# Performance work log

Hardware: AMD Instinct MI355X
Metric: run time of the kernel (lower is better)

## Reference

```python
import jax, jax.numpy as jnp
import numpy as np

WINDOW_SIZE = 20
NEG_BIG = -1e8  # matches -10**8 in the torch mask


def band_mask(S):
    # 0 inside the sliding window |i-j| <= WINDOW_SIZE, -1e8 outside (additive mask)
    idx = jnp.arange(S)
    return jnp.where(jnp.abs(idx[:, None] - idx[None, :]) <= WINDOW_SIZE, 0.0, NEG_BIG).astype(jnp.float32)


def setup_inputs() -> dict:
    key = jax.random.key(0)
    k1, k2, k3, k4 = jax.random.split(key, 4)
    B, S, Dq, Dk = 8, 2048, 1024, 1024
    queries = jax.random.normal(k1, (B, S, Dq), dtype=jnp.float32)
    keys = jax.random.normal(k2, (B, S, Dk), dtype=jnp.float32)
    # reduce = nn.Linear(key_dim, query_dim) since key_dim >= query_dim
    lim = 1.0 / np.sqrt(Dk)
    W_reduce = jax.random.uniform(k3, (Dq, Dk), jnp.float32, -lim, lim)
    b_reduce = jax.random.uniform(k4, (Dq,), jnp.float32, -lim, lim)
    return {"queries": queries, "keys": keys, "W_reduce": W_reduce, "b_reduce": b_reduce}


def reference(queries, keys, W_reduce, b_reduce):
    # values default to the ORIGINAL keys (before dim matching)
    values = keys
    # match_dims: reduce keys to query_dim
    keys_r = jnp.einsum('bkd,qd->bkq', keys, W_reduce) + b_reduce  # [B,S,Dq]
    sims = jnp.einsum('bqd,bkd->bqk', queries, keys_r)             # [B,S,S]
    sims = sims + band_mask(queries.shape[1])                      # additive banded window mask
    weights = jax.nn.softmax(sims, axis=-1)
    return jnp.einsum('bqk,bkd->bqd', weights, values)
```

## Files before the change

kernel.cpp:

```cpp
#include <hip/hip_runtime.h>


#define BATCH 8
#define SEQ   2048
#define DIM   1024
#define WIN   20

typedef _Float16 half8 __attribute__((ext_vector_type(8)));
typedef _Float16 half4v __attribute__((ext_vector_type(4)));
typedef float    f32x4 __attribute__((ext_vector_type(4)));

#define LDK 40

__global__ __launch_bounds__(256) void gemm_qw_f16(const float* __restrict__ Q,
                                                   const float* __restrict__ W,
                                                   float* __restrict__ QT) {
    __shared__ _Float16 Asl[128 * LDK];
    __shared__ _Float16 Bsl[128 * LDK];

    const int m0 = blockIdx.x * 128;
    const int n0 = blockIdx.y * 128;
    const int t  = threadIdx.x;
    const int lane = t & 63;
    const int wv   = t >> 6;
    const int wm   = (wv >> 1) * 64;
    const int wn   = (wv & 1) * 64;
    const int l15  = lane & 15;
    const int quad = lane >> 4;

    const int ar = t >> 1;
    const int ac = (t & 1) * 16;
    const float* Aptr = Q + (size_t)(m0 + ar) * DIM + ac;
    _Float16* AsW = &Asl[ar * LDK + ac];

    const int br = t >> 3;
    const int bc = t & 7;
    const float* Bptr = W + (size_t)br * DIM + n0 + bc;

    f32x4 acc[4][4] = {};

    for (int k0 = 0; k0 < DIM; k0 += 32) {
        float4 a0 = *(const float4*)(Aptr + k0);
        float4 a1 = *(const float4*)(Aptr + k0 + 4);
        float4 a2 = *(const float4*)(Aptr + k0 + 8);
        float4 a3 = *(const float4*)(Aptr + k0 + 12);
        float bv[16];
        #pragma unroll
        for (int j = 0; j < 16; ++j) bv[j] = Bptr[(size_t)k0 * DIM + 8 * j];

        __syncthreads();

        half8 h0, h1;
        h0[0] = (_Float16)a0.x; h0[1] = (_Float16)a0.y; h0[2] = (_Float16)a0.z; h0[3] = (_Float16)a0.w;
        h0[4] = (_Float16)a1.x; h0[5] = (_Float16)a1.y; h0[6] = (_Float16)a1.z; h0[7] = (_Float16)a1.w;
        h1[0] = (_Float16)a2.x; h1[1] = (_Float16)a2.y; h1[2] = (_Float16)a2.z; h1[3] = (_Float16)a2.w;
        h1[4] = (_Float16)a3.x; h1[5] = (_Float16)a3.y; h1[6] = (_Float16)a3.z; h1[7] = (_Float16)a3.w;
        *(half8*)(AsW)     = h0;
        *(half8*)(AsW + 8) = h1;

        #pragma unroll
        for (int j = 0; j < 16; ++j)
            Bsl[(bc + 8 * j) * LDK + br] = (_Float16)bv[j];

        __syncthreads();

        half8 af[4], bf[4];
        #pragma unroll
        for (int i = 0; i < 4; ++i)
            af[i] = *(const half8*)&Asl[(wm + i * 16 + l15) * LDK + quad * 8];
        #pragma unroll
        for (int j = 0; j < 4; ++j)
            bf[j] = *(const half8*)&Bsl[(wn + j * 16 + l15) * LDK + quad * 8];

        #pragma unroll
        for (int i = 0; i < 4; ++i)
            #pragma unroll
            for (int j = 0; j < 4; ++j)
                acc[i][j] = __builtin_amdgcn_mfma_f32_16x16x32_f16(af[i], bf[j], acc[i][j], 0, 0, 0);
    }

    #pragma unroll
    for (int i = 0; i < 4; ++i) {
        const int row0 = m0 + wm + i * 16 + quad * 4;
        #pragma unroll
        for (int r = 0; r < 4; ++r) {
            float* orow = QT + (size_t)(row0 + r) * DIM + n0 + wn + l15;
            #pragma unroll
            for (int j = 0; j < 4; ++j)
                orow[j * 16] = acc[i][j][r];
        }
    }
}

#define TQ  16
#define KP  64
#define KLD 80
#define QLD 80
#define SLD 66

__global__ __launch_bounds__(256, 4) void attn_mfma(const float* __restrict__ QT,
                                                    const float* __restrict__ Keys,
                                                    float* __restrict__ Out) {
    const int blk  = blockIdx.x;
    const int b    = blk & 7;
    const int tile = blk >> 3;
    const int q0   = tile * TQ;
    const int t    = threadIdx.x;
    const int lane = t & 63;
    const int wv   = t >> 6;
    const int l15  = lane & 15;
    const int quad = lane >> 4;

    const int klo = (q0 - WIN) > 0 ? (q0 - WIN) : 0;
    const int khi = (q0 + TQ - 1 + WIN) < (SEQ - 1) ? (q0 + TQ - 1 + WIN) : (SEQ - 1);
    const int nk  = khi - klo + 1;

    const float* qt   = QT + ((size_t)b * SEQ + q0) * DIM;
    const float* keys = Keys + (size_t)b * SEQ * DIM;

    __shared__ _Float16 Qc[TQ * QLD];
    __shared__ _Float16 Ks[KP * KLD];
    __shared__ float    Sl[TQ * SLD];
    __shared__ float    Wl[TQ * SLD];

    const int qr = t >> 4;
    const int qc = (t & 15) * 4;
    const int kr = t >> 2;
    const int kc = (t & 3) * 4;
    const int krow = (klo + kr) < (SEQ - 1) ? (klo + kr) : (SEQ - 1);

    const float* qsrc = qt + (size_t)qr * DIM + qc;
    const float* ksrc = keys + (size_t)krow * DIM + kc;

    f32x4 acc_s = {};

    for (int d0 = 0; d0 < DIM; d0 += 64) {
        float4 qv  = *(const float4*)(qsrc + d0);
        float4 kv0 = *(const float4*)(ksrc + d0);
        float4 kv1 = *(const float4*)(ksrc + d0 + 16);
        float4 kv2 = *(const float4*)(ksrc + d0 + 32);
        float4 kv3 = *(const float4*)(ksrc + d0 + 48);

        __syncthreads();

        half4v hq = {(_Float16)qv.x, (_Float16)qv.y, (_Float16)qv.z, (_Float16)qv.w};
        *(half4v*)&Qc[qr * QLD + qc] = hq;
        half4v h0 = {(_Float16)kv0.x, (_Float16)kv0.y, (_Float16)kv0.z, (_Float16)kv0.w};
        half4v h1 = {(_Float16)kv1.x, (_Float16)kv1.y, (_Float16)kv1.z, (_Float16)kv1.w};
        half4v h2 = {(_Float16)kv2.x, (_Float16)kv2.y, (_Float16)kv2.z, (_Float16)kv2.w};
        half4v h3 = {(_Float16)kv3.x, (_Float16)kv3.y, (_Float16)kv3.z, (_Float16)kv3.w};
        *(half4v*)&Ks[kr * KLD + kc]      = h0;
        *(half4v*)&Ks[kr * KLD + kc + 16] = h1;
        *(half4v*)&Ks[kr * KLD + kc + 32] = h2;
        *(half4v*)&Ks[kr * KLD + kc + 48] = h3;

        __syncthreads();

        #pragma unroll
        for (int s = 0; s < 2; ++s) {
            half8 af = *(const half8*)&Qc[l15 * QLD + s * 32 + quad * 8];
            half8 bf = *(const half8*)&Ks[(wv * 16 + l15) * KLD + s * 32 + quad * 8];
            acc_s = __builtin_amdgcn_mfma_f32_16x16x32_f16(af, bf, acc_s, 0, 0, 0);
        }
    }

    __syncthreads();
    #pragma unroll
    for (int r = 0; r < 4; ++r) {
        const int q = quad * 4 + r;
        const int c = wv * 16 + l15;
        const int d = (q0 + q) - (klo + c);
        const bool valid = (c < nk) && ((unsigned)(d + WIN) <= 2u * WIN);
        Sl[q * SLD + c] = valid ? acc_s[r] : -1e30f;
    }
    __syncthreads();

    if (t < 64) {
        const int q = t >> 2, part = t & 3;
        const float* srow = &Sl[q * SLD + part * 16];
        float*       wrow = &Wl[q * SLD + part * 16];
        float m = -1e30f;
        #pragma unroll
        for (int i = 0; i < 16; ++i) m = fmaxf(m, srow[i]);
        m = fmaxf(m, __shfl_xor(m, 1));
        m = fmaxf(m, __shfl_xor(m, 2));
        float ssum = 0.f;
        #pragma unroll
        for (int i = 0; i < 16; ++i) { float e = expf(srow[i] - m); wrow[i] = e; ssum += e; }
        ssum += __shfl_xor(ssum, 1);
        ssum += __shfl_xor(ssum, 2);
        const float inv = 1.f / ssum;
        #pragma unroll
        for (int i = 0; i < 16; ++i) wrow[i] *= inv;
    }
    __syncthreads();

    float accs[TQ][4] = {};
    for (int c = 0; c < nk; ++c) {
        const float* krow2 = keys + (size_t)(klo + c) * DIM;
        const float k0 = krow2[t], k1 = krow2[t + 256], k2 = krow2[t + 512], k3 = krow2[t + 768];
        #pragma unroll
        for (int q = 0; q < TQ; ++q) {
            const float w = Wl[q * SLD + c];
            accs[q][0] = fmaf(w, k0, accs[q][0]);
            accs[q][1] = fmaf(w, k1, accs[q][1]);
            accs[q][2] = fmaf(w, k2, accs[q][2]);
            accs[q][3] = fmaf(w, k3, accs[q][3]);
        }
    }
    #pragma unroll
    for (int q = 0; q < TQ; ++q) {
        float* orow = Out + ((size_t)b * SEQ + q0 + q) * DIM;
        orow[t]       = accs[q][0];
        orow[t + 256] = accs[q][1];
        orow[t + 512] = accs[q][2];
        orow[t + 768] = accs[q][3];
    }
}

extern "C" void kernel_launch(void* const* d_in, const int* in_sizes, int n_in,
                              void* d_out, int out_size, void* d_ws, size_t ws_size,
                              hipStream_t stream) {
    const float* queries = (const float*)d_in[0];
    const float* keys    = (const float*)d_in[1];
    const float* W       = (const float*)d_in[2];
    float* out = (float*)d_out;

    dim3 g1(128, 8);
    gemm_qw_f16<<<g1, 256, 0, stream>>>(queries, W, out);

    const int nblk = (BATCH * SEQ) / TQ;
    attn_mfma<<<nblk, 256, 0, stream>>>(out, keys, out);
}
```

Baseline: 286.9 us.

## Pre-convert Q and W to fp16 and use swizzled direct-to-LDS GEMM

Adds separate kernels that convert queries to fp16 and transpose-convert W to fp16. A new GEMM then loads both operands straight into LDS through global_load_lds with an XOR swizzle, and writes the Q·W product in fp16 into the workspace. The attention kernel is templated so it can read fp16 QT, which halves its Q traffic. The aim is to cut fp32 load bandwidth and the in-loop conversion and transpose cost in the GEMM. In exchange it adds two extra kernel launches and a full pass over Q, and the fp16 intermediate may cost precision. The old path is kept as a fallback when the workspace is too small.

```diff
diff --git a/kernel.cpp b/kernel.cpp
--- a/kernel.cpp
+++ b/kernel.cpp
@@ -6,12 +6,118 @@
 #define DIM   1024
 #define WIN   20
 
-typedef _Float16 half8 __attribute__((ext_vector_type(8)));
+typedef _Float16 half8  __attribute__((ext_vector_type(8)));
 typedef _Float16 half4v __attribute__((ext_vector_type(4)));
-typedef float    f32x4 __attribute__((ext_vector_type(4)));
+typedef float    f32x4  __attribute__((ext_vector_type(4)));
+
+#define GLOAD_LDS16(gsrc, ldst)                                                        \
+    __builtin_amdgcn_global_load_lds(                                                  \
+        (const __attribute__((address_space(1))) void*)(gsrc),                         \
+        (__attribute__((address_space(3))) void*)(ldst), 16, 0, 0)
+
+__global__ __launch_bounds__(256) void cvt_q_f16(const float* __restrict__ in,
+                                                 _Float16* __restrict__ out) {
+    const int n8 = (BATCH * SEQ * DIM) / 8;
+    for (int i = blockIdx.x * 256 + threadIdx.x; i < n8; i += gridDim.x * 256) {
+        const float4 a = ((const float4*)in)[2 * i];
+        const float4 b = ((const float4*)in)[2 * i + 1];
+        half8 h;
+        h[0] = (_Float16)a.x; h[1] = (_Float16)a.y; h[2] = (_Float16)a.z; h[3] = (_Float16)a.w;
+        h[4] = (_Float16)b.x; h[5] = (_Float16)b.y; h[6] = (_Float16)b.z; h[7] = (_Float16)b.w;
+        ((half8*)out)[i] = h;
+    }
+}
+
+#define WTS 68
+__global__ __launch_bounds__(256) void cvt_w_t(const float* __restrict__ W,
+                                               _Float16* __restrict__ WT) {
+    __shared__ _Float16 tile[64 * WTS];
+    const int k0 = blockIdx.x * 64;
+    const int n0 = blockIdx.y * 64;
+    const int t  = threadIdx.x;
+    const int r  = t >> 4;
+    const int c4 = (t & 15) * 4;
+    #pragma unroll
+    for (int rr = 0; rr < 64; rr += 16) {
+        float4 v = *(const float4*)&W[(size_t)(k0 + rr + r) * DIM + n0 + c4];
+        _Float16* dst = &tile[(rr + r) * WTS + c4];
+        dst[0] = (_Float16)v.x; dst[1] = (_Float16)v.y;
+        dst[2] = (_Float16)v.z; dst[3] = (_Float16)v.w;
+    }
+    __syncthreads();
+    #pragma unroll
+    for (int rr = 0; rr < 64; rr += 16) {
+        const int n = rr + r;
+        half4v h = { tile[(c4 + 0) * WTS + n], tile[(c4 + 1) * WTS + n],
+                     tile[(c4 + 2) * WTS + n], tile[(c4 + 3) * WTS + n] };
+        *(half4v*)&WT[(size_t)(n0 + n) * DIM + k0 + c4] = h;
+    }
+}
+
+#define GK 64
+__global__ __launch_bounds__(256, 2) void gemm_f16t(const _Float16* __restrict__ A,
+                                                    const _Float16* __restrict__ B,
+                                                    _Float16* __restrict__ C) {
+    __shared__ _Float16 As[128 * GK];
+    __shared__ _Float16 Bs[128 * GK];
+
+    const int m0   = blockIdx.x * 128;
+    const int n0   = blockIdx.y * 128;
+    const int t    = threadIdx.x;
+    const int lane = t & 63;
+    const int wv   = t >> 6;
+    const int wm   = (wv >> 1) * 64;
+    const int wn   = (wv & 1) * 64;
+    const int l15  = lane & 15;
+    const int quad = lane >> 4;
+
+    const int srow = lane >> 3;
+    const int sck  = (lane & 7) ^ srow;
+
+    f32x4 acc[4][4] = {};
+
+    for (int k0 = 0; k0 < DIM; k0 += GK) {
+        __syncthreads();
+        #pragma unroll
+        for (int j = 0; j < 4; ++j) {
+            const int rs = (j * 4 + wv) * 8;
+            GLOAD_LDS16(A + (size_t)(m0 + rs + srow) * DIM + k0 + sck * 8, &As[rs * GK]);
+            GLOAD_LDS16(B + (size_t)(n0 + rs + srow) * DIM + k0 + sck * 8, &Bs[rs * GK]);
+        }
+        __syncthreads();
+
+        #pragma unroll
+        for (int s = 0; s < 2; ++s) {
+            half8 af[4], bf[4];
+            #pragma unroll
+            for (int i = 0; i < 4; ++i)
+                af[i] = *(const half8*)&As[(wm + i * 16 + l15) * GK +
+                                           (((s * 4 + quad) ^ (l15 & 7)) * 8)];
+            #pragma unroll
+            for (int j = 0; j < 4; ++j)
+                bf[j] = *(const half8*)&Bs[(wn + j * 16 + l15) * GK +
+                                           (((s * 4 + quad) ^ (l15 & 7)) * 8)];
+            #pragma unroll
+            for (int i = 0; i < 4; ++i)
+                #pragma unroll
+                for (int j = 0; j < 4; ++j)
+                    acc[i][j] = __builtin_amdgcn_mfma_f32_16x16x32_f16(af[i], bf[j], acc[i][j], 0, 0, 0);
+        }
+    }
+
+    #pragma unroll
+    for (int i = 0; i < 4; ++i) {
+        #pragma unroll
+        for (int r = 0; r < 4; ++r) {
+            _Float16* crow = C + (size_t)(m0 + wm + i * 16 + quad * 4 + r) * DIM + n0 + wn + l15;
+            #pragma unroll
+            for (int j = 0; j < 4; ++j)
+                crow[j * 16] = (_Float16)acc[i][j][r];
+        }
+    }
+}
 
 #define LDK 40
-
 __global__ __launch_bounds__(256) void gemm_qw_f16(const float* __restrict__ Q,
                                                    const float* __restrict__ W,
                                                    float* __restrict__ QT) {
@@ -98,7 +204,8 @@
 #define QLD 80
 #define SLD 66
 
-__global__ __launch_bounds__(256, 4) void attn_mfma(const float* __restrict__ QT,
+template <typename QTT>
+__global__ __launch_bounds__(256, 4) void attn_mfma(const QTT* __restrict__ QT,
                                                     const float* __restrict__ Keys,
                                                     float* __restrict__ Out) {
     const int blk  = blockIdx.x;
@@ -115,7 +222,7 @@
     const int khi = (q0 + TQ - 1 + WIN) < (SEQ - 1) ? (q0 + TQ - 1 + WIN) : (SEQ - 1);
     const int nk  = khi - klo + 1;
 
-    const float* qt   = QT + ((size_t)b * SEQ + q0) * DIM;
+    const QTT*   qt   = QT + ((size_t)b * SEQ + q0) * DIM;
     const float* keys = Keys + (size_t)b * SEQ * DIM;
 
     __shared__ _Float16 Qc[TQ * QLD];
@@ -129,13 +236,19 @@
     const int kc = (t & 3) * 4;
     const int krow = (klo + kr) < (SEQ - 1) ? (klo + kr) : (SEQ - 1);
 
-    const float* qsrc = qt + (size_t)qr * DIM + qc;
+    const QTT*   qsrc = qt + (size_t)qr * DIM + qc;
     const float* ksrc = keys + (size_t)krow * DIM + kc;
 
     f32x4 acc_s = {};
 
     for (int d0 = 0; d0 < DIM; d0 += 64) {
-        float4 qv  = *(const float4*)(qsrc + d0);
+        half4v hq;
+        if constexpr (sizeof(QTT) == 2) {
+            hq = *(const half4v*)(qsrc + d0);
+        } else {
+            const float4 qv = *(const float4*)(qsrc + d0);
+            hq = half4v{(_Float16)qv.x, (_Float16)qv.y, (_Float16)qv.z, (_Float16)qv.w};
+        }
         float4 kv0 = *(const float4*)(ksrc + d0);
         float4 kv1 = *(const float4*)(ksrc + d0 + 16);
         float4 kv2 = *(const float4*)(ksrc + d0 + 32);
@@ -143,7 +256,6 @@
 
         __syncthreads();
 
-        half4v hq = {(_Float16)qv.x, (_Float16)qv.y, (_Float16)qv.z, (_Float16)qv.w};
         *(half4v*)&Qc[qr * QLD + qc] = hq;
         half4v h0 = {(_Float16)kv0.x, (_Float16)kv0.y, (_Float16)kv0.z, (_Float16)kv0.w};
         half4v h1 = {(_Float16)kv1.x, (_Float16)kv1.y, (_Float16)kv1.z, (_Float16)kv1.w};
@@ -226,9 +338,21 @@
     const float* W       = (const float*)d_in[2];
     float* out = (float*)d_out;
 
-    dim3 g1(128, 8);
-    gemm_qw_f16<<<g1, 256, 0, stream>>>(queries, W, out);
-
+    const size_t qt16_bytes = (size_t)BATCH * SEQ * DIM * sizeof(_Float16);
+    const size_t w16_bytes  = (size_t)DIM * DIM * sizeof(_Float16);
     const int nblk = (BATCH * SEQ) / TQ;
-    attn_mfma<<<nblk, 256, 0, stream>>>(out, keys, out);
-}
+
+    if (ws_size >= qt16_bytes + w16_bytes) {
+        _Float16* q16  = (_Float16*)d_out;
+        _Float16* qt16 = (_Float16*)d_ws;
+        _Float16* w16t = (_Float16*)((char*)d_ws + qt16_bytes);
+
+        cvt_q_f16<<<2048, 256, 0, stream>>>(queries, q16);
+        cvt_w_t<<<dim3(16, 16), 256, 0, stream>>>(W, w16t);
+        gemm_f16t<<<dim3(128, 8), 256, 0, stream>>>(q16, w16t, qt16);
+        attn_mfma<_Float16><<<nblk, 256, 0, stream>>>(qt16, keys, out);
+    } else {
+        gemm_qw_f16<<<dim3(128, 8), 256, 0, stream>>>(queries, W, out);
+        attn_mfma<float><<<nblk, 256, 0, stream>>>(out, keys, out);
+    }
+}
```

Result: faster. 256.9 us (-10.4%).
